# Kernel optimization log

Hardware: AMD Instinct MI355X
Metric: run time of the kernel (lower is better)

The kernel has to match this reference:

```python
import jax, jax.numpy as jnp
import numpy as np

N = 100000
E = 1600000
EPS = 1e-5  # BatchNorm eps


def setup_inputs() -> dict:
    key = jax.random.key(0)
    ks = jax.random.split(key, 8)
    x = jax.random.normal(ks[0], (N, 8), jnp.float32)
    edge_index = jax.random.randint(ks[1], (2, E), 0, N, dtype=jnp.int64)

    def lin(k, i, o):
        return jax.random.normal(k, (i, o), jnp.float32) / np.float32(np.sqrt(i))

    d = {
        'x': x, 'edge_index': edge_index,
        'W1': lin(ks[2], 8, 64),  'b1': jnp.zeros((64,), jnp.float32),
        'g1': jnp.ones((64,), jnp.float32), 'be1': jnp.zeros((64,), jnp.float32),
        'rm1': jnp.zeros((64,), jnp.float32), 'rv1': jnp.ones((64,), jnp.float32),
        'W2': lin(ks[3], 64, 64), 'b2': jnp.zeros((64,), jnp.float32),
        'g2': jnp.ones((64,), jnp.float32), 'be2': jnp.zeros((64,), jnp.float32),
        'rm2': jnp.zeros((64,), jnp.float32), 'rv2': jnp.ones((64,), jnp.float32),
        'W3': lin(ks[4], 64, 32), 'b3': jnp.zeros((32,), jnp.float32),
        'g3': jnp.ones((32,), jnp.float32), 'be3': jnp.zeros((32,), jnp.float32),
        'rm3': jnp.zeros((32,), jnp.float32), 'rv3': jnp.ones((32,), jnp.float32),
        'Wc': lin(ks[5], 32, 2),  'bc': jnp.zeros((2,), jnp.float32),
    }
    return d


def _gcn_conv(x, W, b, src, dst):
    # PyG GCNConv (improved=False): add self-loops with weight 1, symmetric norm.
    h = x @ W                                               # [N, out]
    deg = jax.ops.segment_sum(jnp.ones((E,), x.dtype), dst, num_segments=N) + 1.0
    dinv = jax.lax.rsqrt(deg)                               # deg >= 1 (self loop)
    norm = dinv[src] * dinv[dst]                            # [E]
    agg = jax.ops.segment_sum(h[src] * norm[:, None], dst, num_segments=N)
    agg = agg + h * (dinv * dinv)[:, None]                  # self-loop messages
    return agg + b


def _bn_eval(x, g, be, rm, rv):
    return (x - rm) * jax.lax.rsqrt(rv + EPS) * g + be


def reference(x, edge_index,
              W1, b1, g1, be1, rm1, rv1,
              W2, b2, g2, be2, rm2, rv2,
              W3, b3, g3, be3, rm3, rv3,
              Wc, bc):
    src, dst = edge_index[0], edge_index[1]
    h = jax.nn.relu(_bn_eval(_gcn_conv(x, W1, b1, src, dst), g1, be1, rm1, rv1))
    h = jax.nn.relu(_bn_eval(_gcn_conv(h, W2, b2, src, dst), g2, be2, rm2, rv2))
    h = jax.nn.relu(_bn_eval(_gcn_conv(h, W3, b3, src, dst), g3, be3, rm3, rv3))
    logits = h @ Wc + bc                                    # [N, 2]
    return jax.nn.log_softmax(logits, axis=-1)
```

## Files before the change

kernel.cpp:

```cpp
#include <hip/hip_runtime.h>
#include <hip/hip_fp16.h>

#define BN_EPS 1e-5f
#define BCAP 5120
#define EDCAP_H64 640
#define EDCAP_CLS 1280

__device__ __forceinline__ unsigned f2u(float a, float b) {
  __half2 h = __floats2half2_rn(a, b);
  return *reinterpret_cast<unsigned*>(&h);
}
__device__ __forceinline__ __half2 uh2(unsigned u) {
  return *reinterpret_cast<__half2*>(&u);
}
__device__ __forceinline__ float2 h22f2(__half2 h) { return __half22float2(h); }
__device__ __forceinline__ __half2 h2shfl_xor(__half2 v, int m) {
  int i = *reinterpret_cast<int*>(&v);
  i = __shfl_xor(i, m);
  return *reinterpret_cast<__half2*>(&i);
}

__global__ void prep(const float* __restrict__ b1, const float* __restrict__ g1,
                     const float* __restrict__ be1, const float* __restrict__ rm1,
                     const float* __restrict__ rv1,
                     const float* __restrict__ b2, const float* __restrict__ g2,
                     const float* __restrict__ be2, const float* __restrict__ rm2,
                     const float* __restrict__ rv2,
                     const float* __restrict__ b3, const float* __restrict__ g3,
                     const float* __restrict__ be3, const float* __restrict__ rm3,
                     const float* __restrict__ rv3,
                     float* __restrict__ bn, int* __restrict__ bcur, int NB) {
  if (blockIdx.x == 0) {
    const int t = threadIdx.x;
    if (t < 64) {
      const float s = g1[t] * rsqrtf(rv1[t] + BN_EPS);
      bn[t] = s;
      bn[64 + t] = (b1[t] - rm1[t]) * s + be1[t];
    } else if (t < 128) {
      const int c = t - 64;
      const float s = g2[c] * rsqrtf(rv2[c] + BN_EPS);
      bn[128 + c] = s;
      bn[192 + c] = (b2[c] - rm2[c]) * s + be2[c];
    } else if (t < 160) {
      const int c = t - 128;
      const float s = g3[c] * rsqrtf(rv3[c] + BN_EPS);
      bn[256 + c] = s;
      bn[288 + c] = (b3[c] - rm3[c]) * s + be3[c];
    }
  } else {
    const int i = (blockIdx.x - 1) * 256 + threadIdx.x;
    if (i <= NB) bcur[i] = 0;
  }
}

__global__ void p1_partition(const int* __restrict__ ei, int* __restrict__ bucketbuf,
                             int* __restrict__ bcur, int E_, int NB) {
  __shared__ int pk[4096];
  __shared__ short bk[4096];
  __shared__ int hist[512];
  __shared__ int bbase[512];
  const int tid = threadIdx.x;
  const int e0 = blockIdx.x * 4096;
  const int ecount = min(4096, E_ - e0);
  for (int i = tid; i < NB; i += 256) hist[i] = 0;
  __syncthreads();
  for (int i = tid; i < ecount; i += 256) {
    const int s = ei[e0 + i];
    const int d = ei[(size_t)E_ + e0 + i];
    pk[i] = ((d & 255) << 24) | s;
    const int b = d >> 8;
    bk[i] = (short)b;
    atomicAdd(&hist[b], 1);
  }
  __syncthreads();
  for (int i = tid; i < NB; i += 256) {
    const int c = hist[i];
    bbase[i] = c ? atomicAdd(&bcur[i], c) : 0;
    hist[i] = 0;
  }
  __syncthreads();
  for (int i = tid; i < ecount; i += 256) {
    const int b = bk[i];
    const int slot = bbase[b] + atomicAdd(&hist[b], 1);
    bucketbuf[(size_t)b * BCAP + slot] = pk[i];
  }
}

__global__ void p2_sort(const int* __restrict__ bucketbuf, const int* __restrict__ bcur,
                        int* __restrict__ gcursor, int* __restrict__ edata,
                        int* __restrict__ rbeg, int* __restrict__ rend,
                        float* __restrict__ dinv, const float* __restrict__ x,
                        __half2* __restrict__ xs, int N_) {
  __shared__ int cntl[256];
  __shared__ int scn[256];
  __shared__ int cur[256];
  __shared__ float dinvl[256];
  __shared__ int sbuf[BCAP];
  __shared__ int sbase;
  const int b = blockIdx.x;
  const int tid = threadIdx.x;
  const int m = bcur[b];
  const int* srcp = bucketbuf + (size_t)b * BCAP;
  cntl[tid] = 0;
  __syncthreads();
  for (int i = tid; i < m; i += 256) atomicAdd(&cntl[(unsigned)srcp[i] >> 24], 1);
  __syncthreads();
  if (tid == 0) sbase = atomicAdd(gcursor, m);
  const int cnt = cntl[tid];
  scn[tid] = cnt;
  __syncthreads();
  for (int off = 1; off < 256; off <<= 1) {
    int u = (tid >= off) ? scn[tid - off] : 0;
    __syncthreads();
    scn[tid] += u;
    __syncthreads();
  }
  const int excl = scn[tid] - cnt;
  cur[tid] = excl;
  const int base = sbase;
  const int node = (b << 8) + tid;
  const float dn = rsqrtf((float)cnt + 1.0f);
  dinvl[tid] = dn;
  if (node < N_) {
    rbeg[node] = base + excl;
    rend[node] = base + excl + cnt;
    dinv[node] = dn;
  }
  __syncthreads();
  for (int i = tid; i < m; i += 256) {
    const int v = srcp[i];
    const int slot = atomicAdd(&cur[(unsigned)v >> 24], 1);
    sbuf[slot] = v & 0xFFFFFF;
  }
  __syncthreads();
  for (int i = tid; i < m; i += 256) edata[(size_t)base + i] = sbuf[i];
  const int nb0 = b << 8;
  for (int i = tid; i < 1024; i += 256) {
    const int nd = nb0 + (i >> 2);
    if (nd < N_) {
      const float d2 = dinvl[i >> 2];
      const float2 v2 = reinterpret_cast<const float2*>(x)[(size_t)nd * 4 + (i & 3)];
      xs[(size_t)nd * 4 + (i & 3)] = __floats2half2_rn(v2.x * d2, v2.y * d2);
    }
  }
}

__global__ void l12(const __half* __restrict__ xs, const float* __restrict__ dinv,
                    const int* __restrict__ rbeg, const int* __restrict__ rend,
                    const int* __restrict__ edata, const float* __restrict__ W1,
                    const float* __restrict__ W2, const float* __restrict__ bn,
                    __half* __restrict__ h2, int n) {
  __shared__ float shw1[8 * 64];
  __shared__ float shagg[32][8];
  __shared__ __half2 sht1[32 * 33];
  __shared__ uint4 shw2[32 * 16];
  const int tid = threadIdx.x;
  const int node0 = blockIdx.x * 32;
  for (int i = tid; i < 512; i += 256) shw1[i] = W1[i];
  {
    __half2* shw2h = reinterpret_cast<__half2*>(shw2);
    for (int i = tid; i < 32 * 64; i += 256) {
      const int kp = i >> 6, c = i & 63;
      shw2h[kp * 64 + c] = __floats2half2_rn(W2[(2 * kp) * 64 + c], W2[(2 * kp + 1) * 64 + c]);
    }
  }
  const int lane = tid & 63;
  const int nl = ((tid >> 6) << 3) + (lane >> 3);
  const int grp = lane & 7;
  const int node = node0 + nl;
  if (node < n) {
    const int beg = rbeg[node], end = rend[node];
    const uint4* xv = reinterpret_cast<const uint4*>(xs);
    __half2 c0 = __half2{0, 0}, c1 = c0, c2 = c0, c3 = c0;
    int e = beg + grp;
    for (; e + 8 < end; e += 16) {
      const uint4 q0 = xv[edata[e]];
      const uint4 q1 = xv[edata[e + 8]];
      c0 = __hadd2(c0, uh2(q0.x)); c1 = __hadd2(c1, uh2(q0.y));
      c2 = __hadd2(c2, uh2(q0.z)); c3 = __hadd2(c3, uh2(q0.w));
      c0 = __hadd2(c0, uh2(q1.x)); c1 = __hadd2(c1, uh2(q1.y));
      c2 = __hadd2(c2, uh2(q1.z)); c3 = __hadd2(c3, uh2(q1.w));
    }
    if (e < end) {
      const uint4 q = xv[edata[e]];
      c0 = __hadd2(c0, uh2(q.x)); c1 = __hadd2(c1, uh2(q.y));
      c2 = __hadd2(c2, uh2(q.z)); c3 = __hadd2(c3, uh2(q.w));
    }
#pragma unroll
    for (int m = 1; m <= 4; m <<= 1) {
      c0 = __hadd2(c0, h2shfl_xor(c0, m));
      c1 = __hadd2(c1, h2shfl_xor(c1, m));
      c2 = __hadd2(c2, h2shfl_xor(c2, m));
      c3 = __hadd2(c3, h2shfl_xor(c3, m));
    }
    if (grp == 0) {
      const uint4 q = xv[node];
      c0 = __hadd2(c0, uh2(q.x)); c1 = __hadd2(c1, uh2(q.y));
      c2 = __hadd2(c2, uh2(q.z)); c3 = __hadd2(c3, uh2(q.w));
      const float dn = dinv[node];
      const float2 f0 = h22f2(c0), f1 = h22f2(c1);
      const float2 f2 = h22f2(c2), f3 = h22f2(c3);
      shagg[nl][0] = f0.x * dn; shagg[nl][1] = f0.y * dn;
      shagg[nl][2] = f1.x * dn; shagg[nl][3] = f1.y * dn;
      shagg[nl][4] = f2.x * dn; shagg[nl][5] = f2.y * dn;
      shagg[nl][6] = f3.x * dn; shagg[nl][7] = f3.y * dn;
    }
  }
  __syncthreads();
  {
    const int mn = tid >> 3;
    const int c = (tid & 7) * 8;
    if (node0 + mn < n) {
      float a[8] = {0, 0, 0, 0, 0, 0, 0, 0};
#pragma unroll
      for (int k = 0; k < 8; ++k) {
        const float s = shagg[mn][k];
#pragma unroll
        for (int j = 0; j < 8; ++j) a[j] += s * shw1[k * 64 + c + j];
      }
      float v[8];
#pragma unroll
      for (int j = 0; j < 8; ++j) {
        float t = a[j] * bn[c + j] + bn[64 + c + j];
        v[j] = t > 0.0f ? t : 0.0f;
      }
#pragma unroll
      for (int j = 0; j < 4; ++j)
        sht1[mn * 33 + (tid & 7) * 4 + j] = __floats2half2_rn(v[2 * j], v[2 * j + 1]);
    }
  }
  __syncthreads();
  const int cq = tid & 15;
  const int nbs = (tid >> 4) * 2;
  float acc[2][4];
#pragma unroll
  for (int j = 0; j < 2; ++j)
#pragma unroll
    for (int k = 0; k < 4; ++k) acc[j][k] = 0.0f;
  for (int kp = 0; kp < 32; ++kp) {
    const uint4 wq = shw2[kp * 16 + cq];
    const float2 w0 = h22f2(uh2(wq.x)), w1 = h22f2(uh2(wq.y));
    const float2 w2 = h22f2(uh2(wq.z)), w3 = h22f2(uh2(wq.w));
#pragma unroll
    for (int j = 0; j < 2; ++j) {
      const float2 s = h22f2(sht1[(nbs + j) * 33 + kp]);
      acc[j][0] += s.x * w0.x + s.y * w0.y;
      acc[j][1] += s.x * w1.x + s.y * w1.y;
      acc[j][2] += s.x * w2.x + s.y * w2.y;
      acc[j][3] += s.x * w3.x + s.y * w3.y;
    }
  }
#pragma unroll
  for (int j = 0; j < 2; ++j) {
    const int nd = node0 + nbs + j;
    if (nd < n) {
      const float dn = dinv[nd];
      uint2 o;
      o.x = f2u(acc[j][0] * dn, acc[j][1] * dn);
      o.y = f2u(acc[j][2] * dn, acc[j][3] * dn);
      reinterpret_cast<uint2*>(h2)[(size_t)nd * 16 + cq] = o;
    }
  }
}

__global__ void gh64_mm3(const __half* __restrict__ h, const float* __restrict__ dinv,
                         const int* __restrict__ rbeg, const int* __restrict__ rend,
                         const int* __restrict__ edata, const float* __restrict__ W3,
                         const float* __restrict__ bn, __half* __restrict__ h3, int n) {
  __shared__ int se[EDCAP_H64];
  __shared__ __half2 shagg2[16 * 33];
  __shared__ __half2 shw3[32 * 32];
  __shared__ float shbn[128];
  const int tid = threadIdx.x;
  const int node0 = blockIdx.x * 16;
  const int last = min(node0 + 15, n - 1);
  const int gb = rbeg[node0];
  const int total = rend[last] - gb;
  const bool lds = (total <= EDCAP_H64);
  if (lds) {
    for (int i = tid; i < total; i += 256) se[i] = edata[gb + i];
  }
  for (int i = tid; i < 32 * 32; i += 256) {
    const int kp = i >> 5, c = i & 31;
    shw3[kp * 32 + c] = __floats2half2_rn(W3[(2 * kp) * 32 + c], W3[(2 * kp + 1) * 32 + c]);
  }
  if (tid < 128) shbn[tid] = bn[128 + tid];
  __syncthreads();
  const int lane = tid & 63;
  const int node = node0 + ((tid >> 6) << 2) + (lane >> 4);
  const int sub = lane & 15;
  const int qi = sub & 7;
  const int grp = sub >> 3;
  if (node < n) {
    const uint4* hv = reinterpret_cast<const uint4*>(h);
    __half2 c0 = __half2{0, 0}, c1 = c0, c2 = c0, c3 = c0;
    if (lds) {
      const int lbeg = rbeg[node] - gb, lend = rend[node] - gb;
      int e = lbeg + grp;
      for (; e + 6 < lend; e += 8) {
        const int s0 = se[e], s1 = se[e + 2], s2 = se[e + 4], s3 = se[e + 6];
        const uint4 q0 = hv[(size_t)s0 * 8 + qi];
        const uint4 q1 = hv[(size_t)s1 * 8 + qi];
        const uint4 q2 = hv[(size_t)s2 * 8 + qi];
        const uint4 q3 = hv[(size_t)s3 * 8 + qi];
        c0 = __hadd2(c0, uh2(q0.x)); c1 = __hadd2(c1, uh2(q0.y));
        c2 = __hadd2(c2, uh2(q0.z)); c3 = __hadd2(c3, uh2(q0.w));
        c0 = __hadd2(c0, uh2(q1.x)); c1 = __hadd2(c1, uh2(q1.y));
        c2 = __hadd2(c2, uh2(q1.z)); c3 = __hadd2(c3, uh2(q1.w));
        c0 = __hadd2(c0, uh2(q2.x)); c1 = __hadd2(c1, uh2(q2.y));
        c2 = __hadd2(c2, uh2(q2.z)); c3 = __hadd2(c3, uh2(q2.w));
        c0 = __hadd2(c0, uh2(q3.x)); c1 = __hadd2(c1, uh2(q3.y));
        c2 = __hadd2(c2, uh2(q3.z)); c3 = __hadd2(c3, uh2(q3.w));
      }
      for (; e < lend; e += 2) {
        const uint4 q = hv[(size_t)se[e] * 8 + qi];
        c0 = __hadd2(c0, uh2(q.x)); c1 = __hadd2(c1, uh2(q.y));
        c2 = __hadd2(c2, uh2(q.z)); c3 = __hadd2(c3, uh2(q.w));
      }
    } else {
      const int beg = rbeg[node], end = rend[node];
      for (int e = beg + grp; e < end; e += 2) {
        const uint4 q = hv[(size_t)edata[e] * 8 + qi];
        c0 = __hadd2(c0, uh2(q.x)); c1 = __hadd2(c1, uh2(q.y));
        c2 = __hadd2(c2, uh2(q.z)); c3 = __hadd2(c3, uh2(q.w));
      }
    }
    c0 = __hadd2(c0, h2shfl_xor(c0, 8));
    c1 = __hadd2(c1, h2shfl_xor(c1, 8));
    c2 = __hadd2(c2, h2shfl_xor(c2, 8));
    c3 = __hadd2(c3, h2shfl_xor(c3, 8));
    if (grp == 0) {
      const uint4 q = hv[(size_t)node * 8 + qi];
      c0 = __hadd2(c0, uh2(q.x)); c1 = __hadd2(c1, uh2(q.y));
      c2 = __hadd2(c2, uh2(q.z)); c3 = __hadd2(c3, uh2(q.w));
      const float dn = dinv[node];
      const int nl = node - node0;
      const float2 f[4] = {h22f2(c0), h22f2(c1), h22f2(c2), h22f2(c3)};
#pragma unroll
      for (int j = 0; j < 4; ++j) {
        const int ch = qi * 8 + 2 * j;
        float v0 = f[j].x * dn * shbn[ch] + shbn[64 + ch];
        float v1 = f[j].y * dn * shbn[ch + 1] + shbn[64 + ch + 1];
        v0 = v0 > 0.0f ? v0 : 0.0f;
        v1 = v1 > 0.0f ? v1 : 0.0f;
        shagg2[nl * 33 + qi * 4 + j] = __floats2half2_rn(v0, v1);
      }
    }
  }
  __syncthreads();
  const int c = tid & 31;
#pragma unroll
  for (int j = 0; j < 2; ++j) {
    const int nl = (tid >> 5) + 8 * j;
    const int mnode = node0 + nl;
    float acc = 0.0f;
#pragma unroll 8
    for (int kp = 0; kp < 32; ++kp) {
      const float2 s = h22f2(shagg2[nl * 33 + kp]);
      const float2 w = h22f2(shw3[kp * 32 + c]);
      acc += s.x * w.x + s.y * w.y;
    }
    float outv = 0.0f;
    if (mnode < n) outv = acc * dinv[mnode];
    const float partner = __shfl_xor(outv, 1);
    if ((c & 1) == 0 && mnode < n) {
      reinterpret_cast<unsigned*>(h3)[(size_t)mnode * 16 + (c >> 1)] = f2u(outv, partner);
    }
  }
}

__global__ void gather_cls(const __half* __restrict__ h, const float* __restrict__ dinv,
                           const int* __restrict__ rbeg, const int* __restrict__ rend,
                           const int* __restrict__ edata, const float* __restrict__ bn,
                           const float* __restrict__ Wc, const float* __restrict__ bc,
                           float* __restrict__ out, int n) {
  __shared__ int se[EDCAP_CLS];
  const int tid = threadIdx.x;
  const int node0 = blockIdx.x * 16;
  const int last = min(node0 + 15, n - 1);
  const int gb = rbeg[node0];
  const int total = rend[last] - gb;
  const bool lds = (total <= EDCAP_CLS);
  if (lds) {
    for (int i = tid; i < total; i += 256) se[i] = edata[gb + i];
  }
  __syncthreads();
  const int lane = tid & 63;
  const int node = node0 + ((tid >> 6) << 2) + (lane >> 4);
  if (node >= n) return;
  const int qi = lane & 3;
  const int grp = (lane >> 2) & 3;
  const uint4* hv = reinterpret_cast<const uint4*>(h);
  __half2 c0 = __half2{0, 0}, c1 = c0, c2 = c0, c3 = c0;
  if (lds) {
    const int beg = rbeg[node] - gb, end = rend[node] - gb;
    int e = beg + grp;
    for (; e + 12 < end; e += 16) {
      const int s0 = se[e], s1 = se[e + 4], s2 = se[e + 8], s3 = se[e + 12];
      const uint4 q0 = hv[(size_t)s0 * 4 + qi];
      const uint4 q1 = hv[(size_t)s1 * 4 + qi];
      const uint4 q2 = hv[(size_t)s2 * 4 + qi];
      const uint4 q3 = hv[(size_t)s3 * 4 + qi];
      c0 = __hadd2(c0, uh2(q0.x)); c1 = __hadd2(c1, uh2(q0.y));
      c2 = __hadd2(c2, uh2(q0.z)); c3 = __hadd2(c3, uh2(q0.w));
      c0 = __hadd2(c0, uh2(q1.x)); c1 = __hadd2(c1, uh2(q1.y));
      c2 = __hadd2(c2, uh2(q1.z)); c3 = __hadd2(c3, uh2(q1.w));
      c0 = __hadd2(c0, uh2(q2.x)); c1 = __hadd2(c1, uh2(q2.y));
      c2 = __hadd2(c2, uh2(q2.z)); c3 = __hadd2(c3, uh2(q2.w));
      c0 = __hadd2(c0, uh2(q3.x)); c1 = __hadd2(c1, uh2(q3.y));
      c2 = __hadd2(c2, uh2(q3.z)); c3 = __hadd2(c3, uh2(q3.w));
    }
    for (; e < end; e += 4) {
      const uint4 q = hv[(size_t)se[e] * 4 + qi];
      c0 = __hadd2(c0, uh2(q.x)); c1 = __hadd2(c1, uh2(q.y));
      c2 = __hadd2(c2, uh2(q.z)); c3 = __hadd2(c3, uh2(q.w));
    }
  } else {
    const int beg = rbeg[node], end = rend[node];
    int e = beg + grp;
    for (; e + 12 < end; e += 16) {
      const int s0 = edata[e], s1 = edata[e + 4], s2 = edata[e + 8], s3 = edata[e + 12];
      const uint4 q0 = hv[(size_t)s0 * 4 + qi];
      const uint4 q1 = hv[(size_t)s1 * 4 + qi];
      const uint4 q2 = hv[(size_t)s2 * 4 + qi];
      const uint4 q3 = hv[(size_t)s3 * 4 + qi];
      c0 = __hadd2(c0, uh2(q0.x)); c1 = __hadd2(c1, uh2(q0.y));
      c2 = __hadd2(c2, uh2(q0.z)); c3 = __hadd2(c3, uh2(q0.w));
      c0 = __hadd2(c0, uh2(q1.x)); c1 = __hadd2(c1, uh2(q1.y));
      c2 = __hadd2(c2, uh2(q1.z)); c3 = __hadd2(c3, uh2(q1.w));
      c0 = __hadd2(c0, uh2(q2.x)); c1 = __hadd2(c1, uh2(q2.y));
      c2 = __hadd2(c2, uh2(q2.z)); c3 = __hadd2(c3, uh2(q2.w));
      c0 = __hadd2(c0, uh2(q3.x)); c1 = __hadd2(c1, uh2(q3.y));
      c2 = __hadd2(c2, uh2(q3.z)); c3 = __hadd2(c3, uh2(q3.w));
    }
    for (; e < end; e += 4) {
      const uint4 q = hv[(size_t)edata[e] * 4 + qi];
      c0 = __hadd2(c0, uh2(q.x)); c1 = __hadd2(c1, uh2(q.y));
      c2 = __hadd2(c2, uh2(q.z)); c3 = __hadd2(c3, uh2(q.w));
    }
  }
#pragma unroll
  for (int m = 4; m <= 8; m <<= 1) {
    c0 = __hadd2(c0, h2shfl_xor(c0, m));
    c1 = __hadd2(c1, h2shfl_xor(c1, m));
    c2 = __hadd2(c2, h2shfl_xor(c2, m));
    c3 = __hadd2(c3, h2shfl_xor(c3, m));
  }
  if (grp != 0) return;
  {
    const uint4 q = hv[(size_t)node * 4 + qi];
    c0 = __hadd2(c0, uh2(q.x)); c1 = __hadd2(c1, uh2(q.y));
    c2 = __hadd2(c2, uh2(q.z)); c3 = __hadd2(c3, uh2(q.w));
  }
  const float dn = dinv[node];
  const float2 f0 = h22f2(c0), f1 = h22f2(c1);
  const float2 f2 = h22f2(c2), f3 = h22f2(c3);
  const float v[8] = {f0.x * dn, f0.y * dn, f1.x * dn, f1.y * dn,
                      f2.x * dn, f2.y * dn, f3.x * dn, f3.y * dn};
  float l0 = 0.0f, l1 = 0.0f;
#pragma unroll
  for (int j = 0; j < 8; ++j) {
    const int c = qi * 8 + j;
    float t = v[j] * bn[256 + c] + bn[288 + c];
    t = t > 0.0f ? t : 0.0f;
    const float2 w = *reinterpret_cast<const float2*>(&Wc[c * 2]);
    l0 += t * w.x;
    l1 += t * w.y;
  }
  l0 += __shfl_xor(l0, 1); l1 += __shfl_xor(l1, 1);
  l0 += __shfl_xor(l0, 2); l1 += __shfl_xor(l1, 2);
  if (qi == 0) {
    l0 += bc[0];
    l1 += bc[1];
    const float m = fmaxf(l0, l1);
    const float lse = m + log1pf(expf(-fabsf(l0 - l1)));
    *reinterpret_cast<float2*>(&out[(size_t)node * 2]) = make_float2(l0 - lse, l1 - lse);
  }
}

extern "C" void kernel_launch(void* const* d_in, const int* in_sizes, int n_in,
                              void* d_out, int out_size, void* d_ws, size_t ws_size,
                              hipStream_t stream) {
  const float* x  = (const float*)d_in[0];
  const int* ei   = (const int*)d_in[1];
  const float* W1 = (const float*)d_in[2];
  const float* b1 = (const float*)d_in[3];
  const float* g1 = (const float*)d_in[4];
  const float* be1 = (const float*)d_in[5];
  const float* rm1 = (const float*)d_in[6];
  const float* rv1 = (const float*)d_in[7];
  const float* W2 = (const float*)d_in[8];
  const float* b2 = (const float*)d_in[9];
  const float* g2 = (const float*)d_in[10];
  const float* be2 = (const float*)d_in[11];
  const float* rm2 = (const float*)d_in[12];
  const float* rv2 = (const float*)d_in[13];
  const float* W3 = (const float*)d_in[14];
  const float* b3 = (const float*)d_in[15];
  const float* g3 = (const float*)d_in[16];
  const float* be3 = (const float*)d_in[17];
  const float* rm3 = (const float*)d_in[18];
  const float* rv3 = (const float*)d_in[19];
  const float* Wc = (const float*)d_in[20];
  const float* bc = (const float*)d_in[21];

  const int N_ = in_sizes[0] / 8;
  const int E_ = in_sizes[1] / 2;
  const int NB = (N_ + 255) >> 8;

  auto align = [](size_t v) { return (v + 255) & ~(size_t)255; };
  char* ws = (char*)d_ws;
  size_t off = 0;
  float* dinv   = (float*)(ws + off); off += align((size_t)N_ * 4);
  int* bcur     = (int*)(ws + off);   off += align(((size_t)NB + 1) * 4);
  int* rbeg     = (int*)(ws + off);   off += align((size_t)N_ * 4);
  int* rend     = (int*)(ws + off);   off += align((size_t)N_ * 4);
  float* bnbuf  = (float*)(ws + off); off += align(320 * 4);
  int* edata    = (int*)(ws + off);   off += align((size_t)E_ * 4);
  __half* xs    = (__half*)(ws + off); off += align((size_t)N_ * 8 * 2);
  char* regionA = ws + off;           off += align((size_t)NB * BCAP * 4);
  char* regionB = ws + off;           off += align((size_t)N_ * 64 * 2);

  int* bucketbuf = (int*)regionA;
  __half* h3   = (__half*)regionA;
  __half* h2   = (__half*)regionB;
  int* gcursor = bcur + NB;

  prep<<<1 + (NB + 1 + 255) / 256, 256, 0, stream>>>(b1, g1, be1, rm1, rv1,
                                                     b2, g2, be2, rm2, rv2,
                                                     b3, g3, be3, rm3, rv3, bnbuf, bcur, NB);
  p1_partition<<<(E_ + 4095) / 4096, 256, 0, stream>>>(ei, bucketbuf, bcur, E_, NB);
  p2_sort<<<NB, 256, 0, stream>>>(bucketbuf, bcur, gcursor, edata, rbeg, rend,
                                  dinv, x, (__half2*)xs, N_);

  l12<<<(N_ + 31) / 32, 256, 0, stream>>>(xs, dinv, rbeg, rend, edata, W1, W2, bnbuf, h2, N_);

  gh64_mm3<<<(N_ + 15) / 16, 256, 0, stream>>>(h2, dinv, rbeg, rend, edata, W3, bnbuf, h3, N_);

  gather_cls<<<(N_ + 15) / 16, 256, 0, stream>>>(h3, dinv, rbeg, rend, edata,
                                                 bnbuf, Wc, bc, (float*)d_out, N_);
}
```

Measured before the change: 147.5 us.

## Precompute half-precision W2/W3 once, vectorize edge loads, widen sort blocks

The W2 and W3 fp16 pair-packing moves into the prep kernel, which writes it once to workspace. The l12 and gh64_mm3 blocks then copy it into shared memory with uint4 loads instead of each block converting fp32 weights itself. The partition kernel reads src/dst as int2 pairs, and the per-bucket sort kernel runs with 512 threads instead of 256. The goal is less redundant per-block weight conversion and more parallelism in the preprocessing stages. It adds a little extra workspace and leaves a dead empty loop in gh64_mm3.

```diff
diff --git a/kernel.cpp b/kernel.cpp
--- a/kernel.cpp
+++ b/kernel.cpp
@@ -29,7 +29,9 @@
                      const float* __restrict__ b3, const float* __restrict__ g3,
                      const float* __restrict__ be3, const float* __restrict__ rm3,
                      const float* __restrict__ rv3,
-                     float* __restrict__ bn, int* __restrict__ bcur, int NB) {
+                     const float* __restrict__ W2, const float* __restrict__ W3,
+                     float* __restrict__ bn, __half2* __restrict__ w2h,
+                     __half2* __restrict__ w3h, int* __restrict__ bcur, int NB) {
   if (blockIdx.x == 0) {
     const int t = threadIdx.x;
     if (t < 64) {
@@ -47,6 +49,14 @@
       bn[256 + c] = s;
       bn[288 + c] = (b3[c] - rm3[c]) * s + be3[c];
     }
+    for (int i = t; i < 2048; i += 256) {
+      const int kp = i >> 6, c = i & 63;
+      w2h[i] = __floats2half2_rn(W2[(2 * kp) * 64 + c], W2[(2 * kp + 1) * 64 + c]);
+    }
+    for (int i = t; i < 1024; i += 256) {
+      const int kp = i >> 5, c = i & 31;
+      w3h[i] = __floats2half2_rn(W3[(2 * kp) * 32 + c], W3[(2 * kp + 1) * 32 + c]);
+    }
   } else {
     const int i = (blockIdx.x - 1) * 256 + threadIdx.x;
     if (i <= NB) bcur[i] = 0;
@@ -64,13 +74,28 @@
   const int ecount = min(4096, E_ - e0);
   for (int i = tid; i < NB; i += 256) hist[i] = 0;
   __syncthreads();
-  for (int i = tid; i < ecount; i += 256) {
+  const int epairs = ecount >> 1;
+  const int2* sp = reinterpret_cast<const int2*>(ei + e0);
+  const int2* dp = reinterpret_cast<const int2*>(ei + (size_t)E_ + e0);
+  for (int i = tid; i < epairs; i += 256) {
+    const int2 s2 = sp[i];
+    const int2 d2 = dp[i];
+    const int i0 = 2 * i, i1 = 2 * i + 1;
+    pk[i0] = ((d2.x & 255) << 24) | s2.x;
+    pk[i1] = ((d2.y & 255) << 24) | s2.y;
+    const int b0 = d2.x >> 8, b1_ = d2.y >> 8;
+    bk[i0] = (short)b0;
+    bk[i1] = (short)b1_;
+    atomicAdd(&hist[b0], 1);
+    atomicAdd(&hist[b1_], 1);
+  }
+  if ((ecount & 1) && tid == 0) {
+    const int i = ecount - 1;
     const int s = ei[e0 + i];
     const int d = ei[(size_t)E_ + e0 + i];
     pk[i] = ((d & 255) << 24) | s;
-    const int b = d >> 8;
-    bk[i] = (short)b;
-    atomicAdd(&hist[b], 1);
+    bk[i] = (short)(d >> 8);
+    atomicAdd(&hist[d >> 8], 1);
   }
   __syncthreads();
   for (int i = tid; i < NB; i += 256) {
@@ -101,41 +126,43 @@
   const int tid = threadIdx.x;
   const int m = bcur[b];
   const int* srcp = bucketbuf + (size_t)b * BCAP;
-  cntl[tid] = 0;
-  __syncthreads();
-  for (int i = tid; i < m; i += 256) atomicAdd(&cntl[(unsigned)srcp[i] >> 24], 1);
+  if (tid < 256) cntl[tid] = 0;
+  __syncthreads();
+  for (int i = tid; i < m; i += 512) atomicAdd(&cntl[(unsigned)srcp[i] >> 24], 1);
   __syncthreads();
   if (tid == 0) sbase = atomicAdd(gcursor, m);
-  const int cnt = cntl[tid];
-  scn[tid] = cnt;
+  const int cnt = (tid < 256) ? cntl[tid] : 0;
+  if (tid < 256) scn[tid] = cnt;
   __syncthreads();
   for (int off = 1; off < 256; off <<= 1) {
-    int u = (tid >= off) ? scn[tid - off] : 0;
+    const int u = (tid < 256 && tid >= off) ? scn[tid - off] : 0;
     __syncthreads();
-    scn[tid] += u;
+    if (tid < 256) scn[tid] += u;
     __syncthreads();
   }
-  const int excl = scn[tid] - cnt;
-  cur[tid] = excl;
   const int base = sbase;
-  const int node = (b << 8) + tid;
-  const float dn = rsqrtf((float)cnt + 1.0f);
-  dinvl[tid] = dn;
-  if (node < N_) {
-    rbeg[node] = base + excl;
-    rend[node] = base + excl + cnt;
-    dinv[node] = dn;
-  }
-  __syncthreads();
-  for (int i = tid; i < m; i += 256) {
+  if (tid < 256) {
+    const int excl = scn[tid] - cnt;
+    cur[tid] = excl;
+    const int node = (b << 8) + tid;
+    const float dn = rsqrtf((float)cnt + 1.0f);
+    dinvl[tid] = dn;
+    if (node < N_) {
+      rbeg[node] = base + excl;
+      rend[node] = base + excl + cnt;
+      dinv[node] = dn;
+    }
+  }
+  __syncthreads();
+  for (int i = tid; i < m; i += 512) {
     const int v = srcp[i];
     const int slot = atomicAdd(&cur[(unsigned)v >> 24], 1);
     sbuf[slot] = v & 0xFFFFFF;
   }
   __syncthreads();
-  for (int i = tid; i < m; i += 256) edata[(size_t)base + i] = sbuf[i];
+  for (int i = tid; i < m; i += 512) edata[(size_t)base + i] = sbuf[i];
   const int nb0 = b << 8;
-  for (int i = tid; i < 1024; i += 256) {
+  for (int i = tid; i < 1024; i += 512) {
     const int nd = nb0 + (i >> 2);
     if (nd < N_) {
       const float d2 = dinvl[i >> 2];
@@ -148,7 +175,7 @@
 __global__ void l12(const __half* __restrict__ xs, const float* __restrict__ dinv,
                     const int* __restrict__ rbeg, const int* __restrict__ rend,
                     const int* __restrict__ edata, const float* __restrict__ W1,
-                    const float* __restrict__ W2, const float* __restrict__ bn,
+                    const __half2* __restrict__ w2h, const float* __restrict__ bn,
                     __half* __restrict__ h2, int n) {
   __shared__ float shw1[8 * 64];
   __shared__ float shagg[32][8];
@@ -157,13 +184,8 @@
   const int tid = threadIdx.x;
   const int node0 = blockIdx.x * 32;
   for (int i = tid; i < 512; i += 256) shw1[i] = W1[i];
-  {
-    __half2* shw2h = reinterpret_cast<__half2*>(shw2);
-    for (int i = tid; i < 32 * 64; i += 256) {
-      const int kp = i >> 6, c = i & 63;
-      shw2h[kp * 64 + c] = __floats2half2_rn(W2[(2 * kp) * 64 + c], W2[(2 * kp + 1) * 64 + c]);
-    }
-  }
+  for (int i = tid; i < 512; i += 256)
+    shw2[i] = reinterpret_cast<const uint4*>(w2h)[i];
   const int lane = tid & 63;
   const int nl = ((tid >> 6) << 3) + (lane >> 3);
   const int grp = lane & 7;
@@ -265,7 +287,7 @@
 
 __global__ void gh64_mm3(const __half* __restrict__ h, const float* __restrict__ dinv,
                          const int* __restrict__ rbeg, const int* __restrict__ rend,
-                         const int* __restrict__ edata, const float* __restrict__ W3,
+                         const int* __restrict__ edata, const __half2* __restrict__ w3h,
                          const float* __restrict__ bn, __half* __restrict__ h3, int n) {
   __shared__ int se[EDCAP_H64];
   __shared__ __half2 shagg2[16 * 33];
@@ -280,10 +302,9 @@
   if (lds) {
     for (int i = tid; i < total; i += 256) se[i] = edata[gb + i];
   }
-  for (int i = tid; i < 32 * 32; i += 256) {
-    const int kp = i >> 5, c = i & 31;
-    shw3[kp * 32 + c] = __floats2half2_rn(W3[(2 * kp) * 32 + c], W3[(2 * kp + 1) * 32 + c]);
-  }
+  for (int i = tid; i < 256; i += 256)
+    reinterpret_cast<uint4*>(shw3)[i + tid - tid] = reinterpret_cast<const uint4*>(w3h)[i];
+  for (int i = tid + 256; i < 256; ) { }
   if (tid < 128) shbn[tid] = bn[128 + tid];
   __syncthreads();
   const int lane = tid & 63;
@@ -516,6 +537,8 @@
   int* rbeg     = (int*)(ws + off);   off += align((size_t)N_ * 4);
   int* rend     = (int*)(ws + off);   off += align((size_t)N_ * 4);
   float* bnbuf  = (float*)(ws + off); off += align(320 * 4);
+  __half2* w2h  = (__half2*)(ws + off); off += align(2048 * 4);
+  __half2* w3h  = (__half2*)(ws + off); off += align(1024 * 4);
   int* edata    = (int*)(ws + off);   off += align((size_t)E_ * 4);
   __half* xs    = (__half*)(ws + off); off += align((size_t)N_ * 8 * 2);
   char* regionA = ws + off;           off += align((size_t)NB * BCAP * 4);
@@ -528,14 +551,15 @@
 
   prep<<<1 + (NB + 1 + 255) / 256, 256, 0, stream>>>(b1, g1, be1, rm1, rv1,
                                                      b2, g2, be2, rm2, rv2,
-                                                     b3, g3, be3, rm3, rv3, bnbuf, bcur, NB);
+                                                     b3, g3, be3, rm3, rv3,
+                                                     W2, W3, bnbuf, w2h, w3h, bcur, NB);
   p1_partition<<<(E_ + 4095) / 4096, 256, 0, stream>>>(ei, bucketbuf, bcur, E_, NB);
-  p2_sort<<<NB, 256, 0, stream>>>(bucketbuf, bcur, gcursor, edata, rbeg, rend,
+  p2_sort<<<NB, 512, 0, stream>>>(bucketbuf, bcur, gcursor, edata, rbeg, rend,
                                   dinv, x, (__half2*)xs, N_);
 
-  l12<<<(N_ + 31) / 32, 256, 0, stream>>>(xs, dinv, rbeg, rend, edata, W1, W2, bnbuf, h2, N_);
-
-  gh64_mm3<<<(N_ + 15) / 16, 256, 0, stream>>>(h2, dinv, rbeg, rend, edata, W3, bnbuf, h3, N_);
+  l12<<<(N_ + 31) / 32, 256, 0, stream>>>(xs, dinv, rbeg, rend, edata, W1, w2h, bnbuf, h2, N_);
+
+  gh64_mm3<<<(N_ + 15) / 16, 256, 0, stream>>>(h2, dinv, rbeg, rend, edata, w3h, bnbuf, h3, N_);
 
   gather_cls<<<(N_ + 15) / 16, 256, 0, stream>>>(h3, dinv, rbeg, rend, edata,
                                                  bnbuf, Wc, bc, (float*)d_out, N_);
```

Measured after the change: 138.7 us. 5.9% less time.
